# Optimization experiments

Measured on AMD Instinct MI355X. Metric: run time of the kernel, lower is better.

## Reference

```python
import jax, jax.numpy as jnp
import numpy as np
from jax import lax

DIM = 1024
N_EXPERTS = 64
TOPK = 8
ROUTE_SCALE = 1.0
B = 262144


def setup_inputs() -> dict:
    key = jax.random.key(0)
    kx, kw, kb = jax.random.split(key, 3)
    x = jax.random.normal(kx, (B, DIM), dtype=jnp.float32)
    # nn.Linear(dim, n_experts): weight [E, dim], bias [E]
    bound = 1.0 / np.sqrt(DIM)
    W = jax.random.uniform(kw, (N_EXPERTS, DIM), minval=-bound, maxval=bound, dtype=jnp.float32)
    b = jax.random.uniform(kb, (N_EXPERTS,), minval=-bound, maxval=bound, dtype=jnp.float32)
    return {"x": x, "W": W, "b": b}


def reference(x, W, b):
    # Router linear: [B, dim] x [dim, E] -> [B, E]
    scores = jnp.einsum("bd,ed->be", x, W) + b
    # score_func == 'softmax' (computed in fp32 as in the torch module)
    probs = jax.nn.softmax(scores.astype(jnp.float32), axis=-1)
    # topk + gather (topk values ARE the gathered original scores)
    weights, indices = lax.top_k(probs, TOPK)            # [B, topk] each
    weights = (weights * ROUTE_SCALE).astype(x.dtype)
    # training-time expert usage histogram (replaces the per-expert python loop)
    expert_usage_count = jnp.zeros((N_EXPERTS,), dtype=jnp.float32).at[indices.reshape(-1)].add(1.0)
    total_tokens = jnp.float32(B * TOPK)
    return weights, indices, expert_usage_count, total_tokens
```

## Files before the change

kernel.cpp:

```cpp
#include <hip/hip_runtime.h>
#include <math.h>

#define NTOK   262144
#define DIM    1024
#define NEXP   64
#define TOPK   8
#define ROWS   256
#define BLK    512
#define BK     32
#define NKC    (DIM / BK)
#define SLICE  8512

#define OFF_IDX ((size_t)NTOK * TOPK)
#define OFF_USE (2 * (size_t)NTOK * TOPK)
#define OFF_TOT (OFF_USE + NEXP)

typedef __attribute__((ext_vector_type(8))) short bf16x8;
typedef __attribute__((ext_vector_type(4))) float f32x4;

union FragU { bf16x8 v; unsigned int u[4]; };

__device__ __forceinline__ bf16x8 pack_bf16(float4 a, float4 b) {
    FragU r;
    r.u[0] = (__float_as_uint(a.x) >> 16) | (__float_as_uint(a.y) & 0xFFFF0000u);
    r.u[1] = (__float_as_uint(a.z) >> 16) | (__float_as_uint(a.w) & 0xFFFF0000u);
    r.u[2] = (__float_as_uint(b.x) >> 16) | (__float_as_uint(b.y) & 0xFFFF0000u);
    r.u[3] = (__float_as_uint(b.z) >> 16) | (__float_as_uint(b.w) & 0xFFFF0000u);
    return r.v;
}

__global__ __launch_bounds__(256) void gate_prep_kernel(const float* __restrict__ W,
                                                        unsigned short* __restrict__ wf,
                                                        float* __restrict__ out) {
    int idx = blockIdx.x * 256 + threadIdx.x;
    int j    = idx & 7;
    int lane = (idx >> 3) & 63;
    int nt   = (idx >> 9) & 3;
    int kc   = idx >> 11;
    int fq = lane >> 4, fr = lane & 15;
    float v = W[(size_t)(nt * 16 + fr) * DIM + kc * BK + fq * 8 + j];
    unsigned int u = __float_as_uint(v);
    u += 0x7FFFu + ((u >> 16) & 1u);
    wf[idx] = (unsigned short)(u >> 16);

    if (blockIdx.x == 0) {
        if (threadIdx.x < NEXP) out[OFF_USE + threadIdx.x] = 0.0f;
        if (threadIdx.x == NEXP) out[OFF_TOT] = (float)((size_t)NTOK * TOPK);
    }
}

__global__ __launch_bounds__(BLK, 4) void gate_kernel(const float* __restrict__ x,
                                                      const unsigned short* __restrict__ wf,
                                                      const float* __restrict__ bias,
                                                      float* __restrict__ out) {
    __shared__ __align__(16) char smem[8 * SLICE];
    __shared__ float hist[NEXP];

    const int tid  = threadIdx.x;
    const int w    = tid >> 6;
    const int lane = tid & 63;
    const int fq   = lane >> 4;
    const int fr   = lane & 15;
    const size_t rowBase = (size_t)blockIdx.x * ROWS;

    if (tid < NEXP) hist[tid] = 0.0f;

    char* myslice = smem + w * SLICE;

    const char* xb = (const char*)(x + (rowBase + (size_t)w * 32) * DIM);
    const char* src[4];
#pragma unroll
    for (int i = 0; i < 4; i++) {
        int flat = i * 64 + lane;
        int row = flat >> 3, sp = flat & 7;
        src[i] = xb + (size_t)row * (DIM * 4) + (sp ^ (row & 7)) * 16;
    }

#define STAGE(BUF, kc)                                                            \
    do {                                                                          \
        _Pragma("unroll")                                                         \
        for (int i_ = 0; i_ < 4; i_++)                                            \
            __builtin_amdgcn_global_load_lds(                                     \
                (const __attribute__((address_space(1))) unsigned int*)(src[i_] + (kc) * 128), \
                (__attribute__((address_space(3))) unsigned int*)(myslice + (BUF) * 4096 + i_ * 1024), \
                16, 0, 0);                                                        \
    } while (0)

    const int c   = fr & 7;
    const int a00 = fr * 8 + ((fq * 2) ^ c);
    const int a01 = fr * 8 + ((fq * 2 + 1) ^ c);
    const int a10 = (fr + 16) * 8 + ((fq * 2) ^ c);
    const int a11 = (fr + 16) * 8 + ((fq * 2 + 1) ^ c);

    const bf16x8* wfv = (const bf16x8*)wf;

    f32x4 acc[2][4] = {};
    bf16x8 bcur[4];

#pragma unroll
    for (int nt = 0; nt < 4; nt++) bcur[nt] = wfv[(size_t)nt * 64 + lane];
    STAGE(0, 0);

#define GSTEP(kc, BUF, PREF)                                                      \
    {                                                                             \
        bf16x8 bnext[4];                                                          \
        if (PREF) {                                                               \
            _Pragma("unroll")                                                     \
            for (int nt = 0; nt < 4; nt++)                                        \
                bnext[nt] = wfv[(size_t)(((kc) + 1) * 4 + nt) * 64 + lane];       \
            STAGE((BUF) ^ 1, (kc) + 1);                                           \
            asm volatile("s_waitcnt vmcnt(8)" ::: "memory");                      \
        } else {                                                                  \
            asm volatile("s_waitcnt vmcnt(0)" ::: "memory");                      \
        }                                                                         \
        __builtin_amdgcn_sched_barrier(0);                                        \
        const float4* xt = (const float4*)(myslice + (BUF) * 4096);               \
        bf16x8 af0 = pack_bf16(xt[a00], xt[a01]);                                 \
        bf16x8 af1 = pack_bf16(xt[a10], xt[a11]);                                 \
        _Pragma("unroll")                                                         \
        for (int nt = 0; nt < 4; nt++) {                                          \
            acc[0][nt] = __builtin_amdgcn_mfma_f32_16x16x32_bf16(af0, bcur[nt], acc[0][nt], 0, 0, 0); \
            acc[1][nt] = __builtin_amdgcn_mfma_f32_16x16x32_bf16(af1, bcur[nt], acc[1][nt], 0, 0, 0); \
        }                                                                         \
        if (PREF) {                                                               \
            _Pragma("unroll")                                                     \
            for (int nt = 0; nt < 4; nt++) bcur[nt] = bnext[nt];                  \
        }                                                                         \
    }

    for (int kc = 0; kc < NKC - 2; kc += 2) {
        GSTEP(kc, 0, 1);
        GSTEP(kc + 1, 1, 1);
    }
    GSTEP(NKC - 2, 0, 1);
    GSTEP(NKC - 1, 1, 0);

    float* sw = (float*)myslice;
    float bv[4];
#pragma unroll
    for (int nt = 0; nt < 4; nt++) bv[nt] = bias[nt * 16 + fr];
#pragma unroll
    for (int mt = 0; mt < 2; mt++) {
        int mbase = mt * 16 + fq * 4;
#pragma unroll
        for (int nt = 0; nt < 4; nt++) {
            int n = nt * 16 + fr;
#pragma unroll
            for (int r = 0; r < 4; r++)
                sw[(mbase + r) * 65 + n] = acc[mt][nt][r] + bv[nt];
        }
    }
    __syncthreads();

    if (tid < ROWS) {
        const float* rp = (const float*)(smem + (tid >> 5) * SLICE) + (tid & 31) * 65;
        float m = rp[0];
#pragma unroll 8
        for (int e = 1; e < NEXP; e++) m = fmaxf(m, rp[e]);

        float tv[8]; int ti[8];
#pragma unroll
        for (int k = 0; k < 8; k++) { tv[k] = -1.0f; ti[k] = 0; }
        float sum = 0.0f;

#pragma unroll 4
        for (int e = 0; e < NEXP; e++) {
            float ev = __expf(rp[e] - m);
            sum += ev;
#pragma unroll
            for (int k = 7; k >= 1; k--) {
                bool up   = ev > tv[k - 1];
                bool here = ev > tv[k];
                float nv = up ? tv[k - 1] : (here ? ev : tv[k]);
                int   ni = up ? ti[k - 1] : (here ? e : ti[k]);
                tv[k] = nv; ti[k] = ni;
            }
            bool c0 = ev > tv[0];
            ti[0] = c0 ? e : ti[0];
            tv[0] = c0 ? ev : tv[0];
        }
        float rinv = 1.0f / sum;

        size_t ro = (rowBase + tid) * TOPK;
        *(float4*)(out + ro)     = make_float4(tv[0] * rinv, tv[1] * rinv, tv[2] * rinv, tv[3] * rinv);
        *(float4*)(out + ro + 4) = make_float4(tv[4] * rinv, tv[5] * rinv, tv[6] * rinv, tv[7] * rinv);
        *(float4*)(out + OFF_IDX + ro)     = make_float4((float)ti[0], (float)ti[1], (float)ti[2], (float)ti[3]);
        *(float4*)(out + OFF_IDX + ro + 4) = make_float4((float)ti[4], (float)ti[5], (float)ti[6], (float)ti[7]);
#pragma unroll
        for (int k = 0; k < 8; k++) atomicAdd(&hist[ti[k]], 1.0f);
    }
    __syncthreads();
    if (tid < NEXP) atomicAdd(&out[OFF_USE + tid], hist[tid]);
}

extern "C" void kernel_launch(void* const* d_in, const int* in_sizes, int n_in,
                              void* d_out, int out_size, void* d_ws, size_t ws_size,
                              hipStream_t stream) {
    const float* x    = (const float*)d_in[0];
    const float* W    = (const float*)d_in[1];
    const float* bias = (const float*)d_in[2];
    float* out = (float*)d_out;
    unsigned short* wf = (unsigned short*)d_ws;

    gate_prep_kernel<<<256, 256, 0, stream>>>(W, wf, out);
    gate_kernel<<<NTOK / ROWS, BLK, 0, stream>>>(x, wf, bias, out);
}
```

Measured before the change: 254.6 us.

## Shrink per-wave row tile to 16 rows and widen K slab to 64

Each wave now handles 16 token rows instead of 32, and each staged slab covers 64 K-elements, with a 16-slot XOR swizzle and two k-steps per slab. Blocks process 128 rows, so the grid is twice as large and there are half as many pipeline iterations per wave. The goal is more blocks in flight and fewer waitcnt/barrier stalls per unit of K. The cost is that each wave reuses its W fragments across only one 16-row tile instead of two, which doubles the W traffic per token and raises register use for the 8 B fragments.

```diff
diff --git a/kernel.cpp b/kernel.cpp
--- a/kernel.cpp
+++ b/kernel.cpp
@@ -5,11 +5,12 @@
 #define DIM    1024
 #define NEXP   64
 #define TOPK   8
-#define ROWS   256
+#define WROWS  16
+#define ROWS   128
 #define BLK    512
-#define BK     32
-#define NKC    (DIM / BK)
-#define SLICE  8512
+#define BKF    64
+#define NSLAB  (DIM / BKF)
+#define SLICE  8192
 
 #define OFF_IDX ((size_t)NTOK * TOPK)
 #define OFF_USE (2 * (size_t)NTOK * TOPK)
@@ -38,7 +39,7 @@
     int nt   = (idx >> 9) & 3;
     int kc   = idx >> 11;
     int fq = lane >> 4, fr = lane & 15;
-    float v = W[(size_t)(nt * 16 + fr) * DIM + kc * BK + fq * 8 + j];
+    float v = W[(size_t)(nt * 16 + fr) * DIM + kc * 32 + fq * 8 + j];
     unsigned int u = __float_as_uint(v);
     u += 0x7FFFu + ((u >> 16) & 1u);
     wf[idx] = (unsigned short)(u >> 16);
@@ -67,93 +68,89 @@
 
     char* myslice = smem + w * SLICE;
 
-    const char* xb = (const char*)(x + (rowBase + (size_t)w * 32) * DIM);
+    const char* xb = (const char*)(x + (rowBase + (size_t)w * WROWS) * DIM);
     const char* src[4];
 #pragma unroll
     for (int i = 0; i < 4; i++) {
         int flat = i * 64 + lane;
-        int row = flat >> 3, sp = flat & 7;
-        src[i] = xb + (size_t)row * (DIM * 4) + (sp ^ (row & 7)) * 16;
-    }
-
-#define STAGE(BUF, kc)                                                            \
+        int row = flat >> 4;
+        int u = (flat & 15) ^ row;
+        src[i] = xb + (size_t)row * (DIM * 4) + u * 16;
+    }
+
+#define STAGE(BUF, slab)                                                          \
     do {                                                                          \
         _Pragma("unroll")                                                         \
         for (int i_ = 0; i_ < 4; i_++)                                            \
             __builtin_amdgcn_global_load_lds(                                     \
-                (const __attribute__((address_space(1))) unsigned int*)(src[i_] + (kc) * 128), \
+                (const __attribute__((address_space(1))) unsigned int*)(src[i_] + (slab) * 256), \
                 (__attribute__((address_space(3))) unsigned int*)(myslice + (BUF) * 4096 + i_ * 1024), \
                 16, 0, 0);                                                        \
     } while (0)
 
-    const int c   = fr & 7;
-    const int a00 = fr * 8 + ((fq * 2) ^ c);
-    const int a01 = fr * 8 + ((fq * 2 + 1) ^ c);
-    const int a10 = (fr + 16) * 8 + ((fq * 2) ^ c);
-    const int a11 = (fr + 16) * 8 + ((fq * 2 + 1) ^ c);
+    int aslot[2][2];
+#pragma unroll
+    for (int kk = 0; kk < 2; kk++)
+#pragma unroll
+        for (int h = 0; h < 2; h++)
+            aslot[kk][h] = fr * 16 + (((kk * 8 + fq * 2 + h) ^ fr) & 15);
 
     const bf16x8* wfv = (const bf16x8*)wf;
 
-    f32x4 acc[2][4] = {};
-    bf16x8 bcur[4];
-
-#pragma unroll
-    for (int nt = 0; nt < 4; nt++) bcur[nt] = wfv[(size_t)nt * 64 + lane];
+    f32x4 acc[4] = {};
+    bf16x8 bcur[8];
+
+#pragma unroll
+    for (int f = 0; f < 8; f++) bcur[f] = wfv[(size_t)f * 64 + lane];
     STAGE(0, 0);
 
-#define GSTEP(kc, BUF, PREF)                                                      \
+#define GSLAB(slab, BUF, PREF)                                                    \
     {                                                                             \
-        bf16x8 bnext[4];                                                          \
+        bf16x8 bnext[8];                                                          \
         if (PREF) {                                                               \
             _Pragma("unroll")                                                     \
-            for (int nt = 0; nt < 4; nt++)                                        \
-                bnext[nt] = wfv[(size_t)(((kc) + 1) * 4 + nt) * 64 + lane];       \
-            STAGE((BUF) ^ 1, (kc) + 1);                                           \
-            asm volatile("s_waitcnt vmcnt(8)" ::: "memory");                      \
+            for (int f = 0; f < 8; f++)                                           \
+                bnext[f] = wfv[(size_t)(((slab) + 1) * 8 + f) * 64 + lane];       \
+            STAGE((BUF) ^ 1, (slab) + 1);                                         \
+            asm volatile("s_waitcnt vmcnt(12)" ::: "memory");                     \
         } else {                                                                  \
             asm volatile("s_waitcnt vmcnt(0)" ::: "memory");                      \
         }                                                                         \
         __builtin_amdgcn_sched_barrier(0);                                        \
         const float4* xt = (const float4*)(myslice + (BUF) * 4096);               \
-        bf16x8 af0 = pack_bf16(xt[a00], xt[a01]);                                 \
-        bf16x8 af1 = pack_bf16(xt[a10], xt[a11]);                                 \
         _Pragma("unroll")                                                         \
-        for (int nt = 0; nt < 4; nt++) {                                          \
-            acc[0][nt] = __builtin_amdgcn_mfma_f32_16x16x32_bf16(af0, bcur[nt], acc[0][nt], 0, 0, 0); \
-            acc[1][nt] = __builtin_amdgcn_mfma_f32_16x16x32_bf16(af1, bcur[nt], acc[1][nt], 0, 0, 0); \
+        for (int kk = 0; kk < 2; kk++) {                                          \
+            bf16x8 af = pack_bf16(xt[aslot[kk][0]], xt[aslot[kk][1]]);            \
+            _Pragma("unroll")                                                     \
+            for (int nt = 0; nt < 4; nt++)                                        \
+                acc[nt] = __builtin_amdgcn_mfma_f32_16x16x32_bf16(af, bcur[kk * 4 + nt], acc[nt], 0, 0, 0); \
         }                                                                         \
         if (PREF) {                                                               \
             _Pragma("unroll")                                                     \
-            for (int nt = 0; nt < 4; nt++) bcur[nt] = bnext[nt];                  \
+            for (int f = 0; f < 8; f++) bcur[f] = bnext[f];                       \
         }                                                                         \
     }
 
-    for (int kc = 0; kc < NKC - 2; kc += 2) {
-        GSTEP(kc, 0, 1);
-        GSTEP(kc + 1, 1, 1);
-    }
-    GSTEP(NKC - 2, 0, 1);
-    GSTEP(NKC - 1, 1, 0);
+    for (int s = 0; s < NSLAB - 1; ++s) {
+        GSLAB(s, s & 1, 1);
+    }
+    GSLAB(NSLAB - 1, (NSLAB - 1) & 1, 0);
 
     float* sw = (float*)myslice;
     float bv[4];
 #pragma unroll
     for (int nt = 0; nt < 4; nt++) bv[nt] = bias[nt * 16 + fr];
 #pragma unroll
-    for (int mt = 0; mt < 2; mt++) {
-        int mbase = mt * 16 + fq * 4;
-#pragma unroll
-        for (int nt = 0; nt < 4; nt++) {
-            int n = nt * 16 + fr;
-#pragma unroll
-            for (int r = 0; r < 4; r++)
-                sw[(mbase + r) * 65 + n] = acc[mt][nt][r] + bv[nt];
-        }
+    for (int nt = 0; nt < 4; nt++) {
+        int n = nt * 16 + fr;
+#pragma unroll
+        for (int r = 0; r < 4; r++)
+            sw[(fq * 4 + r) * 65 + n] = acc[nt][r] + bv[nt];
     }
     __syncthreads();
 
     if (tid < ROWS) {
-        const float* rp = (const float*)(smem + (tid >> 5) * SLICE) + (tid & 31) * 65;
+        const float* rp = (const float*)(smem + (tid >> 4) * SLICE) + (tid & 15) * 65;
         float m = rp[0];
 #pragma unroll 8
         for (int e = 1; e < NEXP; e++) m = fmaxf(m, rp[e]);
```

Result: slower. 261.9 us (+2.8%).

## Use 256-thread blocks with 64 rows per wave and top-k on raw scores

Applied to the files above, without the earlier changes.

Each block now runs 4 waves instead of 8, and each wave handles 64 token rows (4 M-tiles) instead of 32. Every B fragment of W loaded from global is therefore reused across twice as many MFMAs, and all 256 threads do the softmax/top-k epilogue rather than half of them. The top-k selection now runs on raw logits, with the max taken from the first selected value. The full exp-sum is a separate pass and exp is applied only to the 8 selected values. The cost is more accumulator registers, a larger LDS slice per wave and fewer resident waves (launch bound 2), which can reduce latency hiding for this memory-bound stream of x.

```diff
diff --git a/kernel.cpp b/kernel.cpp
--- a/kernel.cpp
+++ b/kernel.cpp
@@ -5,11 +5,12 @@
 #define DIM    1024
 #define NEXP   64
 #define TOPK   8
+#define WROWS  64
 #define ROWS   256
-#define BLK    512
+#define BLK    256
 #define BK     32
 #define NKC    (DIM / BK)
-#define SLICE  8512
+#define SLICE  16896
 
 #define OFF_IDX ((size_t)NTOK * TOPK)
 #define OFF_USE (2 * (size_t)NTOK * TOPK)
@@ -49,11 +50,11 @@
     }
 }
 
-__global__ __launch_bounds__(BLK, 4) void gate_kernel(const float* __restrict__ x,
+__global__ __launch_bounds__(BLK, 2) void gate_kernel(const float* __restrict__ x,
                                                       const unsigned short* __restrict__ wf,
                                                       const float* __restrict__ bias,
                                                       float* __restrict__ out) {
-    __shared__ __align__(16) char smem[8 * SLICE];
+    __shared__ __align__(16) char smem[4 * SLICE];
     __shared__ float hist[NEXP];
 
     const int tid  = threadIdx.x;
@@ -67,34 +68,36 @@
 
     char* myslice = smem + w * SLICE;
 
-    const char* xb = (const char*)(x + (rowBase + (size_t)w * 32) * DIM);
-    const char* src[4];
-#pragma unroll
-    for (int i = 0; i < 4; i++) {
+    const char* xb = (const char*)(x + (rowBase + (size_t)w * WROWS) * DIM);
+    const char* src[8];
+#pragma unroll
+    for (int i = 0; i < 8; i++) {
         int flat = i * 64 + lane;
-        int row = flat >> 3, sp = flat & 7;
-        src[i] = xb + (size_t)row * (DIM * 4) + (sp ^ (row & 7)) * 16;
+        int row = flat >> 3;
+        int u = (flat & 7) ^ (row & 7);
+        src[i] = xb + (size_t)row * (DIM * 4) + u * 16;
     }
 
 #define STAGE(BUF, kc)                                                            \
     do {                                                                          \
         _Pragma("unroll")                                                         \
-        for (int i_ = 0; i_ < 4; i_++)                                            \
+        for (int i_ = 0; i_ < 8; i_++)                                            \
             __builtin_amdgcn_global_load_lds(                                     \
                 (const __attribute__((address_space(1))) unsigned int*)(src[i_] + (kc) * 128), \
-                (__attribute__((address_space(3))) unsigned int*)(myslice + (BUF) * 4096 + i_ * 1024), \
+                (__attribute__((address_space(3))) unsigned int*)(myslice + (BUF) * 8192 + i_ * 1024), \
                 16, 0, 0);                                                        \
     } while (0)
 
-    const int c   = fr & 7;
-    const int a00 = fr * 8 + ((fq * 2) ^ c);
-    const int a01 = fr * 8 + ((fq * 2 + 1) ^ c);
-    const int a10 = (fr + 16) * 8 + ((fq * 2) ^ c);
-    const int a11 = (fr + 16) * 8 + ((fq * 2 + 1) ^ c);
+    int aslot[4][2];
+#pragma unroll
+    for (int mt = 0; mt < 4; mt++)
+#pragma unroll
+        for (int h = 0; h < 2; h++)
+            aslot[mt][h] = (mt * 16 + fr) * 8 + (((fq * 2 + h) ^ fr) & 7);
 
     const bf16x8* wfv = (const bf16x8*)wf;
 
-    f32x4 acc[2][4] = {};
+    f32x4 acc[4][4] = {};
     bf16x8 bcur[4];
 
 #pragma unroll
@@ -109,18 +112,18 @@
             for (int nt = 0; nt < 4; nt++)                                        \
                 bnext[nt] = wfv[(size_t)(((kc) + 1) * 4 + nt) * 64 + lane];       \
             STAGE((BUF) ^ 1, (kc) + 1);                                           \
-            asm volatile("s_waitcnt vmcnt(8)" ::: "memory");                      \
+            asm volatile("s_waitcnt vmcnt(12)" ::: "memory");                     \
         } else {                                                                  \
             asm volatile("s_waitcnt vmcnt(0)" ::: "memory");                      \
         }                                                                         \
         __builtin_amdgcn_sched_barrier(0);                                        \
-        const float4* xt = (const float4*)(myslice + (BUF) * 4096);               \
-        bf16x8 af0 = pack_bf16(xt[a00], xt[a01]);                                 \
-        bf16x8 af1 = pack_bf16(xt[a10], xt[a11]);                                 \
+        const float4* xt = (const float4*)(myslice + (BUF) * 8192);               \
         _Pragma("unroll")                                                         \
-        for (int nt = 0; nt < 4; nt++) {                                          \
-            acc[0][nt] = __builtin_amdgcn_mfma_f32_16x16x32_bf16(af0, bcur[nt], acc[0][nt], 0, 0, 0); \
-            acc[1][nt] = __builtin_amdgcn_mfma_f32_16x16x32_bf16(af1, bcur[nt], acc[1][nt], 0, 0, 0); \
+        for (int mt = 0; mt < 4; mt++) {                                          \
+            bf16x8 af = pack_bf16(xt[aslot[mt][0]], xt[aslot[mt][1]]);            \
+            _Pragma("unroll")                                                     \
+            for (int nt = 0; nt < 4; nt++)                                        \
+                acc[mt][nt] = __builtin_amdgcn_mfma_f32_16x16x32_bf16(af, bcur[nt], acc[mt][nt], 0, 0, 0); \
         }                                                                         \
         if (PREF) {                                                               \
             _Pragma("unroll")                                                     \
@@ -140,7 +143,7 @@
 #pragma unroll
     for (int nt = 0; nt < 4; nt++) bv[nt] = bias[nt * 16 + fr];
 #pragma unroll
-    for (int mt = 0; mt < 2; mt++) {
+    for (int mt = 0; mt < 4; mt++) {
         int mbase = mt * 16 + fq * 4;
 #pragma unroll
         for (int nt = 0; nt < 4; nt++) {
@@ -152,38 +155,42 @@
     }
     __syncthreads();
 
-    if (tid < ROWS) {
-        const float* rp = (const float*)(smem + (tid >> 5) * SLICE) + (tid & 31) * 65;
-        float m = rp[0];
-#pragma unroll 8
-        for (int e = 1; e < NEXP; e++) m = fmaxf(m, rp[e]);
+    {
+        const float* rp = (const float*)(smem + (tid >> 6) * SLICE) + (tid & 63) * 65;
 
         float tv[8]; int ti[8];
 #pragma unroll
-        for (int k = 0; k < 8; k++) { tv[k] = -1.0f; ti[k] = 0; }
-        float sum = 0.0f;
+        for (int k = 0; k < 8; k++) { tv[k] = -1e30f; ti[k] = 0; }
 
 #pragma unroll 4
         for (int e = 0; e < NEXP; e++) {
-            float ev = __expf(rp[e] - m);
-            sum += ev;
+            float s = rp[e];
 #pragma unroll
             for (int k = 7; k >= 1; k--) {
-                bool up   = ev > tv[k - 1];
-                bool here = ev > tv[k];
-                float nv = up ? tv[k - 1] : (here ? ev : tv[k]);
+                bool up   = s > tv[k - 1];
+                bool here = s > tv[k];
+                float nv = up ? tv[k - 1] : (here ? s : tv[k]);
                 int   ni = up ? ti[k - 1] : (here ? e : ti[k]);
                 tv[k] = nv; ti[k] = ni;
             }
-            bool c0 = ev > tv[0];
+            bool c0 = s > tv[0];
             ti[0] = c0 ? e : ti[0];
-            tv[0] = c0 ? ev : tv[0];
+            tv[0] = c0 ? s : tv[0];
         }
+        float m = tv[0];
+
+        float sum = 0.0f;
+#pragma unroll 8
+        for (int e = 0; e < NEXP; e++) sum += __expf(rp[e] - m);
         float rinv = 1.0f / sum;
 
+        float wv_[8];
+#pragma unroll
+        for (int k = 0; k < 8; k++) wv_[k] = __expf(tv[k] - m) * rinv;
+
         size_t ro = (rowBase + tid) * TOPK;
-        *(float4*)(out + ro)     = make_float4(tv[0] * rinv, tv[1] * rinv, tv[2] * rinv, tv[3] * rinv);
-        *(float4*)(out + ro + 4) = make_float4(tv[4] * rinv, tv[5] * rinv, tv[6] * rinv, tv[7] * rinv);
+        *(float4*)(out + ro)     = make_float4(wv_[0], wv_[1], wv_[2], wv_[3]);
+        *(float4*)(out + ro + 4) = make_float4(wv_[4], wv_[5], wv_[6], wv_[7]);
         *(float4*)(out + OFF_IDX + ro)     = make_float4((float)ti[0], (float)ti[1], (float)ti[2], (float)ti[3]);
         *(float4*)(out + OFF_IDX + ro + 4) = make_float4((float)ti[4], (float)ti[5], (float)ti[6], (float)ti[7]);
 #pragma unroll
```

Result: slower. 260.2 us (+2.2%).
